# Performance work log

Hardware: AMD Instinct MI355X
Metric: run time of the kernel (lower is better)

Reference implementation:

```python
import jax, jax.numpy as jnp
import numpy as np

B, N, D, H, K = 8, 128, 256, 128, 8

def setup_inputs() -> dict:
    key = jax.random.key(0)
    ks = jax.random.split(key, 6)
    E = jax.random.normal(ks[0], (B, N, D), dtype=jnp.float32)
    # kaiming_uniform-like init for linear weights
    lim1 = np.sqrt(6.0 / (2 * D))
    W1 = jax.random.uniform(ks[1], (H, 2 * D), minval=-lim1, maxval=lim1, dtype=jnp.float32)
    b1 = jnp.zeros((H,), dtype=jnp.float32)
    lim2 = np.sqrt(6.0 / H)
    W2 = jax.random.uniform(ks[2], (D, H), minval=-lim2, maxval=lim2, dtype=jnp.float32)
    b2 = jnp.zeros((D,), dtype=jnp.float32)
    q = jax.random.normal(ks[3], (K, D), dtype=jnp.float32) * (1.0 / D ** 0.5)
    return {"E": E, "W1": W1, "b1": b1, "W2": W2, "b2": b2, "q": q}

def reference(E, W1, b1, W2, b2, q):
    # phi(cat(Ei,Ej)) == relu(E_i @ W1a^T + E_j @ W1b^T + b1) @ W2^T + b2
    # Split first linear's weight to avoid materializing the [B,N,N,2D] concat.
    W1a, W1b = W1[:, :D], W1[:, D:]          # each [H, D]
    Ai = jnp.einsum('bnd,hd->bnh', E, W1a)   # [B,N,H] (row half)
    Aj = jnp.einsum('bnd,hd->bnh', E, W1b)   # [B,N,H] (col half)
    hidden = jax.nn.relu(Ai[:, :, None, :] + Aj[:, None, :, :] + b1)  # [B,N,N,H]
    # dropout is identity at inference
    # Fuse second linear with query dot: (hidden @ W2^T + b2) . q_h
    #   = hidden @ (W2^T q_h) + b2.q_h
    Wq = jnp.einsum('dh,kd->hk', W2, q)      # [H, K]
    bq = jnp.einsum('d,kd->k', b2, q)        # [K]
    logits = jnp.einsum('bijh,hk->bijh'[:0] or 'bijh,hk->bijk', hidden, Wq) + bq  # [B,N,N,K]
    M = jax.nn.sigmoid(logits).transpose(0, 3, 1, 2)  # [B,K,N,N]
    eye = jnp.eye(N, dtype=M.dtype)[None, None]
    return M * (1.0 - eye)
```

## Files before the change

kernel.cpp:

```cpp
#include <hip/hip_runtime.h>

#define PB 8
#define PN 128
#define PD 256
#define PH 128
#define PK 8
#define D2 (2*PD)
#define NT 4

__global__ __launch_bounds__(128) void t0_prep(
        const float* __restrict__ W1, const float* __restrict__ W2,
        const float* __restrict__ b2, const float* __restrict__ q,
        float* __restrict__ W1t, float* __restrict__ Wq, float* __restrict__ bq)
{
    const int blk = blockIdx.x, t = threadIdx.x;
    if (blk < D2) {
        W1t[blk * PH + t] = W1[t * D2 + blk];
    } else {
        const int k = blk - D2;
        __shared__ float qs[PD];
        __shared__ float red[128];
        qs[t]       = q[k * PD + t];
        qs[t + 128] = q[k * PD + t + 128];
        __syncthreads();
        float acc = 0.f;
        #pragma unroll 4
        for (int d = 0; d < PD; ++d)
            acc = fmaf(W2[d * PH + t], qs[d], acc);
        Wq[t * PK + k] = acc;
        red[t] = b2[t] * qs[t] + b2[t + 128] * qs[t + 128];
        __syncthreads();
        for (int s = 64; s > 0; s >>= 1) { if (t < s) red[t] += red[t + s]; __syncthreads(); }
        if (t == 0) bq[k] = red[0];
    }
}

__global__ __launch_bounds__(256) void k1_proj(
        const float* __restrict__ E, const float* __restrict__ W1t,
        const float* __restrict__ b1,
        float* __restrict__ Ai, float* __restrict__ Ajt)
{
    const int blk = blockIdx.x, t = threadIdx.x;
    const int b  = blk / (PN / NT);
    const int n0 = (blk % (PN / NT)) * NT;
    const int h = t & (PH - 1);
    const int part = t >> 7;

    const float* w = W1t + part * PD * PH + h;
    const float* e = E + (b * PN + n0) * PD;

    float acc[NT];
    #pragma unroll
    for (int n = 0; n < NT; ++n) acc[n] = 0.f;

    #pragma unroll 8
    for (int d = 0; d < PD; ++d) {
        const float wv = w[d * PH];
        #pragma unroll
        for (int n = 0; n < NT; ++n)
            acc[n] = fmaf(wv, e[n * PD + d], acc[n]);
    }

    if (part == 0) {
        const float bb = b1[h];
        #pragma unroll
        for (int n = 0; n < NT; ++n)
            Ai[(b * PN + n0 + n) * PH + h] = acc[n] + bb;
    } else {
        #pragma unroll
        for (int n = 0; n < NT; ++n)
            Ajt[(b * PH + h) * PN + n0 + n] = acc[n];
    }
}

__global__ __launch_bounds__(256) void k2_score(
        const float* __restrict__ Ai, const float* __restrict__ Ajt,
        const float* __restrict__ Wq, const float* __restrict__ bq,
        float* __restrict__ out)
{
    const int blk = blockIdx.x, t = threadIdx.x;
    const int b = blk >> 6;
    const int i = ((blk & 63) << 1) + (t >> 7);
    const int j = t & (PN - 1);

    const float* ai = Ai + (b * PN + i) * PH;
    const float* aj = Ajt + b * PH * PN + j;

    float acc[PK];
    #pragma unroll
    for (int k = 0; k < PK; ++k) acc[k] = bq[k];

    #pragma unroll 4
    for (int h = 0; h < PH; ++h) {
        const float v = fmaxf(ai[h] + aj[h * PN], 0.f);
        #pragma unroll
        for (int k = 0; k < PK; ++k)
            acc[k] = fmaf(v, Wq[h * PK + k], acc[k]);
    }

    #pragma unroll
    for (int k = 0; k < PK; ++k) {
        float s = __builtin_amdgcn_rcpf(1.f + __expf(-acc[k]));
        if (j == i) s = 0.f;
        out[((b * PK + k) * PN + i) * PN + j] = s;
    }
}

extern "C" void kernel_launch(void* const* d_in, const int* in_sizes, int n_in,
                              void* d_out, int out_size, void* d_ws, size_t ws_size,
                              hipStream_t stream) {
    const float* E  = (const float*)d_in[0];
    const float* W1 = (const float*)d_in[1];
    const float* b1 = (const float*)d_in[2];
    const float* W2 = (const float*)d_in[3];
    const float* b2 = (const float*)d_in[4];
    const float* q  = (const float*)d_in[5];

    float* Ai  = (float*)d_ws;
    float* Ajt = Ai + PB * PN * PH;
    float* W1t = Ajt + PB * PN * PH;
    float* Wq  = W1t + D2 * PH;
    float* bq  = Wq + PH * PK;

    t0_prep<<<D2 + PK, 128, 0, stream>>>(W1, W2, b2, q, W1t, Wq, bq);
    k1_proj<<<PB * (PN / NT), 256, 0, stream>>>(E, W1t, b1, Ai, Ajt);
    k2_score<<<PB * PN / 2, 256, 0, stream>>>(Ai, Ajt, Wq, bq, (float*)d_out);
}
```

Measured before the change: 107.5 us.

## Stage operands in shared memory and vectorize loads across all three kernels

The W1 transpose now goes through a padded 32x33 shared tile so both the reads and the writes are coalesced, and it runs on 64 blocks instead of 512. The projection kernel stages the E rows in shared memory, reads them as float4, and writes Ajt with one float4 store per thread. The score kernel stages Wq, its two Ai rows and bq in shared memory and reads Wq as float4. The sigmoid also switches from the fast rcp builtin to a true division, which adds some cost.

```diff
diff --git a/kernel.cpp b/kernel.cpp
--- a/kernel.cpp
+++ b/kernel.cpp
@@ -8,29 +8,40 @@
 #define D2 (2*PD)
 #define NT 4
 
-__global__ __launch_bounds__(128) void t0_prep(
+__global__ __launch_bounds__(256) void t0_prep(
         const float* __restrict__ W1, const float* __restrict__ W2,
         const float* __restrict__ b2, const float* __restrict__ q,
         float* __restrict__ W1t, float* __restrict__ Wq, float* __restrict__ bq)
 {
     const int blk = blockIdx.x, t = threadIdx.x;
-    if (blk < D2) {
-        W1t[blk * PH + t] = W1[t * D2 + blk];
+    if (blk < 64) {
+        __shared__ float tile[32][33];
+        const int h0 = (blk >> 4) << 5;
+        const int d0 = (blk & 15) << 5;
+        const int tx = t & 31, ty = t >> 5;
+        #pragma unroll
+        for (int s = 0; s < 4; ++s)
+            tile[ty + 8 * s][tx] = W1[(h0 + ty + 8 * s) * D2 + d0 + tx];
+        __syncthreads();
+        #pragma unroll
+        for (int s = 0; s < 4; ++s)
+            W1t[(d0 + ty + 8 * s) * PH + h0 + tx] = tile[tx][ty + 8 * s];
     } else {
-        const int k = blk - D2;
+        const int k = blk - 64;
         __shared__ float qs[PD];
-        __shared__ float red[128];
-        qs[t]       = q[k * PD + t];
-        qs[t + 128] = q[k * PD + t + 128];
+        __shared__ float red[256];
+        qs[t] = q[k * PD + t];
         __syncthreads();
-        float acc = 0.f;
-        #pragma unroll 4
-        for (int d = 0; d < PD; ++d)
-            acc = fmaf(W2[d * PH + t], qs[d], acc);
-        Wq[t * PK + k] = acc;
-        red[t] = b2[t] * qs[t] + b2[t + 128] * qs[t + 128];
+        if (t < PH) {
+            float acc = 0.f;
+            #pragma unroll 4
+            for (int d = 0; d < PD; ++d)
+                acc = fmaf(W2[d * PH + t], qs[d], acc);
+            Wq[t * PK + k] = acc;
+        }
+        red[t] = b2[t] * qs[t];
         __syncthreads();
-        for (int s = 64; s > 0; s >>= 1) { if (t < s) red[t] += red[t + s]; __syncthreads(); }
+        for (int s = 128; s > 0; s >>= 1) { if (t < s) red[t] += red[t + s]; __syncthreads(); }
         if (t == 0) bq[k] = red[0];
     }
 }
@@ -40,25 +51,35 @@
         const float* __restrict__ b1,
         float* __restrict__ Ai, float* __restrict__ Ajt)
 {
+    __shared__ float es[NT][PD];
     const int blk = blockIdx.x, t = threadIdx.x;
-    const int b  = blk / (PN / NT);
-    const int n0 = (blk % (PN / NT)) * NT;
+    const int b  = blk >> 5;
+    const int n0 = (blk & 31) * NT;
+
+    const float* erow = E + (b * PN + n0) * PD;
+    #pragma unroll
+    for (int n = 0; n < NT; ++n)
+        es[n][t] = erow[n * PD + t];
+    __syncthreads();
+
     const int h = t & (PH - 1);
     const int part = t >> 7;
+    const float* w = W1t + part * PD * PH + h;
 
-    const float* w = W1t + part * PD * PH + h;
-    const float* e = E + (b * PN + n0) * PD;
-
-    float acc[NT];
-    #pragma unroll
-    for (int n = 0; n < NT; ++n) acc[n] = 0.f;
-
-    #pragma unroll 8
-    for (int d = 0; d < PD; ++d) {
-        const float wv = w[d * PH];
+    float acc[NT] = {0.f, 0.f, 0.f, 0.f};
+    #pragma unroll 4
+    for (int d = 0; d < PD; d += 4) {
+        float wv[4];
         #pragma unroll
-        for (int n = 0; n < NT; ++n)
-            acc[n] = fmaf(wv, e[n * PD + d], acc[n]);
+        for (int r = 0; r < 4; ++r) wv[r] = w[(d + r) * PH];
+        #pragma unroll
+        for (int n = 0; n < NT; ++n) {
+            float4 e4 = *reinterpret_cast<const float4*>(&es[n][d]);
+            acc[n] = fmaf(wv[0], e4.x, acc[n]);
+            acc[n] = fmaf(wv[1], e4.y, acc[n]);
+            acc[n] = fmaf(wv[2], e4.z, acc[n]);
+            acc[n] = fmaf(wv[3], e4.w, acc[n]);
+        }
     }
 
     if (part == 0) {
@@ -67,9 +88,8 @@
         for (int n = 0; n < NT; ++n)
             Ai[(b * PN + n0 + n) * PH + h] = acc[n] + bb;
     } else {
-        #pragma unroll
-        for (int n = 0; n < NT; ++n)
-            Ajt[(b * PH + h) * PN + n0 + n] = acc[n];
+        float4 v = make_float4(acc[0], acc[1], acc[2], acc[3]);
+        *reinterpret_cast<float4*>(&Ajt[(b * PH + h) * PN + n0]) = v;
     }
 }
 
@@ -78,29 +98,44 @@
         const float* __restrict__ Wq, const float* __restrict__ bq,
         float* __restrict__ out)
 {
+    __shared__ float wq[PH * PK];
+    __shared__ float ais[2 * PH];
+    __shared__ float bqs[PK];
+
     const int blk = blockIdx.x, t = threadIdx.x;
-    const int b = blk >> 6;
-    const int i = ((blk & 63) << 1) + (t >> 7);
+    const int b  = blk >> 6;
+    const int i0 = (blk & 63) << 1;
+
+    *reinterpret_cast<float4*>(&wq[t * 4]) =
+        *reinterpret_cast<const float4*>(&Wq[t * 4]);
+    ais[t] = Ai[(b * PN + i0) * PH + t];
+    if (t < PK) bqs[t] = bq[t];
+    __syncthreads();
+
+    const int half = t >> 7;
+    const int i = i0 + half;
     const int j = t & (PN - 1);
-
-    const float* ai = Ai + (b * PN + i) * PH;
+    const float* ail = ais + half * PH;
     const float* aj = Ajt + b * PH * PN + j;
 
     float acc[PK];
     #pragma unroll
-    for (int k = 0; k < PK; ++k) acc[k] = bq[k];
+    for (int k = 0; k < PK; ++k) acc[k] = bqs[k];
 
     #pragma unroll 4
     for (int h = 0; h < PH; ++h) {
-        const float v = fmaxf(ai[h] + aj[h * PN], 0.f);
-        #pragma unroll
-        for (int k = 0; k < PK; ++k)
-            acc[k] = fmaf(v, Wq[h * PK + k], acc[k]);
+        const float v = fmaxf(ail[h] + aj[h * PN], 0.f);
+        float4 w0 = *reinterpret_cast<const float4*>(&wq[h * PK]);
+        float4 w1 = *reinterpret_cast<const float4*>(&wq[h * PK + 4]);
+        acc[0] = fmaf(v, w0.x, acc[0]); acc[1] = fmaf(v, w0.y, acc[1]);
+        acc[2] = fmaf(v, w0.z, acc[2]); acc[3] = fmaf(v, w0.w, acc[3]);
+        acc[4] = fmaf(v, w1.x, acc[4]); acc[5] = fmaf(v, w1.y, acc[5]);
+        acc[6] = fmaf(v, w1.z, acc[6]); acc[7] = fmaf(v, w1.w, acc[7]);
     }
 
     #pragma unroll
     for (int k = 0; k < PK; ++k) {
-        float s = __builtin_amdgcn_rcpf(1.f + __expf(-acc[k]));
+        float s = 1.f / (1.f + __expf(-acc[k]));
         if (j == i) s = 0.f;
         out[((b * PK + k) * PN + i) * PN + j] = s;
     }
@@ -122,7 +157,7 @@
     float* Wq  = W1t + D2 * PH;
     float* bq  = Wq + PH * PK;
 
-    t0_prep<<<D2 + PK, 128, 0, stream>>>(W1, W2, b2, q, W1t, Wq, bq);
+    t0_prep<<<64 + PK, 256, 0, stream>>>(W1, W2, b2, q, W1t, Wq, bq);
     k1_proj<<<PB * (PN / NT), 256, 0, stream>>>(E, W1t, b1, Ai, Ajt);
     k2_score<<<PB * PN / 2, 256, 0, stream>>>(Ai, Ajt, Wq, bq, (float*)d_out);
 }
```

Result: faster. 101.4 us (-5.7%).
